# Kernel tuning notes

Hardware: AMD Instinct MI355X
Metric: run time of the kernel (lower is better)

Reference implementation:

```python
import jax, jax.numpy as jnp
import numpy as np

B, S, D, H, MULT = 4, 2048, 768, 12, 4
HD = D // H
EPS = 1e-6


def _ln(x, g, b):
    mu = jnp.mean(x, axis=-1, keepdims=True)
    var = jnp.var(x, axis=-1, keepdims=True)
    return (x - mu) * jax.lax.rsqrt(var + EPS) * g + b


def setup_inputs() -> dict:
    key = jax.random.key(0)
    ks = jax.random.split(key, 12)
    sd = 0.02
    inp = {
        "x": jax.random.normal(ks[0], (B, S, D), dtype=jnp.float32),
        "mask": jnp.ones((B, 1, 1, S), dtype=jnp.int32),
        "Wq": jax.random.normal(ks[1], (D, D), dtype=jnp.float32) * sd,
        "bq": jnp.zeros((D,), dtype=jnp.float32),
        "Wk": jax.random.normal(ks[2], (D, D), dtype=jnp.float32) * sd,
        "bk": jnp.zeros((D,), dtype=jnp.float32),
        "Wv": jax.random.normal(ks[3], (D, D), dtype=jnp.float32) * sd,
        "bv": jnp.zeros((D,), dtype=jnp.float32),
        "Wo": jax.random.normal(ks[4], (D, D), dtype=jnp.float32) * sd,
        "bo": jnp.zeros((D,), dtype=jnp.float32),
        "W1": jax.random.normal(ks[5], (D, MULT * D), dtype=jnp.float32) * sd,
        "b1": jnp.zeros((MULT * D,), dtype=jnp.float32),
        "W2": jax.random.normal(ks[6], (MULT * D, D), dtype=jnp.float32) * sd,
        "b2": jnp.zeros((D,), dtype=jnp.float32),
        "g1": jnp.ones((D,), dtype=jnp.float32),
        "be1": jnp.zeros((D,), dtype=jnp.float32),
        "g2": jnp.ones((D,), dtype=jnp.float32),
        "be2": jnp.zeros((D,), dtype=jnp.float32),
    }
    return inp


def reference(x, mask, Wq, bq, Wk, bk, Wv, bv, Wo, bo, W1, b1, W2, b2, g1, be1, g2, be2):
    scale = HD ** -0.5
    # projections -> [B,H,S,HD]
    q = (x @ Wq + bq).reshape(B, S, H, HD).transpose(0, 2, 1, 3)
    k = (x @ Wk + bk).reshape(B, S, H, HD).transpose(0, 2, 1, 3)
    v = (x @ Wv + bv).reshape(B, S, H, HD).transpose(0, 2, 1, 3)
    scores = jnp.einsum("bhqd,bhkd->bhqk", q, k) * scale
    scores = jnp.where(mask == 0, -jnp.inf, scores)
    attn = jax.nn.softmax(scores, axis=-1)
    out = jnp.einsum("bhqk,bhkd->bhqd", attn, v)
    out = out.transpose(0, 2, 1, 3).reshape(B, S, D)
    mha = out @ Wo + bo
    # residual + LN
    h = _ln(mha + x, g1, be1)
    # FFN (dropout inactive in eval; GELU exact as torch nn.GELU default)
    ff = jax.nn.gelu(h @ W1 + b1, approximate=False) @ W2 + b2
    return _ln(ff + h, g2, be2)
```

## Files before the change

kernel.cpp:

```cpp
#include <hip/hip_runtime.h>
#include <hip/hip_bf16.h>
#include <math.h>

#define B_  4
#define S_  2048
#define D_  768
#define H_  12
#define HD_ 64
#define DF_ 3072
#define BS_ (B_*S_)

#define QSCALE 0.18033688011112042f

typedef __attribute__((ext_vector_type(8))) short short8;
typedef __attribute__((ext_vector_type(4))) float f32x4;
typedef __attribute__((ext_vector_type(4))) int  int4v;

__device__ __forceinline__ unsigned short f2b(float f){
    unsigned int x = __float_as_uint(f);
    return (unsigned short)((x + 0x7fffu + ((x >> 16) & 1u)) >> 16);
}

typedef __attribute__((address_space(1))) void gvoid_t;
typedef __attribute__((address_space(3))) void lvoid_t;
__device__ __forceinline__ void gload_lds16(const unsigned short* g, unsigned short* l){
    __builtin_amdgcn_global_load_lds((gvoid_t*)g, (lvoid_t*)l, 16, 0, 0);
}

__global__ __launch_bounds__(256) void prep_kernel(
    const float* __restrict__ x,
    const float* __restrict__ Wq, const float* __restrict__ Wk,
    const float* __restrict__ Wv, const float* __restrict__ Wo,
    const float* __restrict__ W1, const float* __restrict__ W2,
    const float* __restrict__ bq, const float* __restrict__ bk, const float* __restrict__ bv,
    unsigned short* __restrict__ xb, unsigned short* __restrict__ wqkvT,
    unsigned short* __restrict__ woT, unsigned short* __restrict__ w1T,
    unsigned short* __restrict__ w2T, float* __restrict__ bqkv)
{
    const int NCVT = (BS_*D_)/256;
    int bid = blockIdx.x;
    if (bid < NCVT){
        int i = bid*256 + threadIdx.x;
        xb[i] = f2b(x[i]);
        return;
    }
    bid -= NCVT;
    __shared__ float t[32][33];
    const float* src; unsigned short* dst; int K, N, bx, by;
    if (bid < 4*576){
        int wsel = bid / 576, tt = bid % 576;
        bx = tt % 24; by = tt / 24; K = D_; N = D_;
        src = (wsel==0)?Wq:(wsel==1)?Wk:(wsel==2)?Wv:Wo;
        dst = (wsel<3) ? (wqkvT + (size_t)wsel*D_*D_) : woT;
    } else if (bid < 4*576 + 2304){
        int tt = bid - 4*576; bx = tt % 96; by = tt / 96; K = D_; N = DF_; src = W1; dst = w1T;
    } else if (bid < 4*576 + 2*2304){
        int tt = bid - 4*576 - 2304; bx = tt % 24; by = tt / 24; K = DF_; N = D_; src = W2; dst = w2T;
    } else {
        int i = (bid - (4*576 + 2*2304))*256 + threadIdx.x;
        if (i < 3*D_) bqkv[i] = (i < D_) ? bq[i] : (i < 2*D_) ? bk[i-D_] : bv[i-2*D_];
        return;
    }
    int tx = threadIdx.x & 31, ty = threadIdx.x >> 5;
    #pragma unroll
    for (int i = 0; i < 4; ++i)
        t[ty + i*8][tx] = src[(size_t)(by*32 + ty + i*8) * N + bx*32 + tx];
    __syncthreads();
    #pragma unroll
    for (int i = 0; i < 4; ++i)
        dst[(size_t)(bx*32 + ty + i*8) * K + by*32 + tx] = f2b(t[tx][ty + i*8]);
}

__global__ __launch_bounds__(256, 3) void gemm_tn(
    const unsigned short* __restrict__ A,
    const unsigned short* __restrict__ Bt,
    const float* __restrict__ bias,
    float* __restrict__ Cf,
    unsigned short* __restrict__ Cb,
    unsigned short* __restrict__ vtg,
    int M, int N, int K, int klen, int act)
{
    __shared__ __align__(16) unsigned short As[128*32];
    __shared__ __align__(16) unsigned short Bs[128*32];

    const int tid  = threadIdx.x;
    const int bm   = blockIdx.y, bn = blockIdx.x, bz = blockIdx.z;
    const int w    = tid >> 6, lane = tid & 63;
    const int l16  = lane & 15, quad = lane >> 4;
    const int wm   = (w >> 1) * 64, wn = (w & 1) * 64;
    const int kbeg = bz * klen;

    const unsigned short* Abase = A  + (size_t)bm * 128 * K;
    const unsigned short* Bbase = Bt + (size_t)bn * 128 * K;

    f32x4 acc[4][4] = {};

    for (int kt = kbeg; kt < kbeg + klen; kt += 32){
        #pragma unroll
        for (int c0 = 0; c0 < 2; ++c0){
            int c = tid + c0 * 256;
            int row = c >> 2, q = c & 3;
            gload_lds16(Abase + (size_t)row * K + kt + q*8, As + c*8);
            gload_lds16(Bbase + (size_t)row * K + kt + q*8, Bs + c*8);
        }
        __syncthreads();

        short8 af[4], bf[4];
        #pragma unroll
        for (int mi = 0; mi < 4; ++mi) af[mi] = *(const short8*)&As[(wm + mi*16 + l16)*32 + quad*8];
        #pragma unroll
        for (int ni = 0; ni < 4; ++ni) bf[ni] = *(const short8*)&Bs[(wn + ni*16 + l16)*32 + quad*8];
        #pragma unroll
        for (int mi = 0; mi < 4; ++mi)
            #pragma unroll
            for (int ni = 0; ni < 4; ++ni)
                acc[mi][ni] = __builtin_amdgcn_mfma_f32_16x16x32_bf16(af[mi], bf[ni], acc[mi][ni], 0, 0, 0);
        __syncthreads();
    }

    if (act == 2 && bn >= 12){
        #pragma unroll
        for (int mi = 0; mi < 4; ++mi){
            int rowbase = bm*128 + wm + mi*16 + quad*4;
            int bidx = rowbase >> 11, s0 = rowbase & 2047;
            int sp = (s0 & ~31) | (((s0 >> 2) & 3) << 3) | (((s0 >> 4) & 1) << 2);
            #pragma unroll
            for (int ni = 0; ni < 4; ++ni){
                int col  = bn*128 + wn + ni*16 + l16;
                int hcol = col - 2*D_;
                int hh   = hcol >> 6, dd = hcol & 63;
                float bia = bias ? bias[col] : 0.f;
                unsigned long long pk = 0;
                #pragma unroll
                for (int r = 0; r < 4; ++r)
                    pk |= (unsigned long long)f2b(acc[mi][ni][r] + bia) << (16*r);
                *(unsigned long long*)(vtg + (((size_t)bidx*H_ + hh)*64 + dd)*2048 + sp) = pk;
            }
        }
        return;
    }

    float* Cfz = Cf ? (Cf + (size_t)bz * M * N) : nullptr;
    const bool addb = (bias != nullptr) && (bz == 0);
    #pragma unroll
    for (int mi = 0; mi < 4; ++mi){
        #pragma unroll
        for (int ni = 0; ni < 4; ++ni){
            int col = bn*128 + wn + ni*16 + l16;
            float bia = addb ? bias[col] : 0.f;
            #pragma unroll
            for (int r = 0; r < 4; ++r){
                int row = bm*128 + wm + mi*16 + quad*4 + r;
                float v = acc[mi][ni][r] + bia;
                if (act == 1){
                    float u = v * (0.7978845608028654f + 0.0356774081f * v * v);
                    float e = __builtin_amdgcn_exp2f(u * 2.885390081777927f);
                    v = 0.5f * v * (1.f + (1.f - 2.f / (e + 1.f)));
                } else if (act == 2 && col < D_) v *= QSCALE;
                size_t idx = (size_t)row * N + col;
                if (Cfz) Cfz[idx] = v;
                if (Cb) Cb[idx] = f2b(v);
            }
        }
    }
}

__global__ __launch_bounds__(256, 2) void attn_kernel(
    const unsigned short* __restrict__ qkv,
    const unsigned short* __restrict__ vtg,
    const int* __restrict__ mask,
    unsigned short* __restrict__ ctx)
{
    __shared__ __align__(16) unsigned short Kl[128*64];
    __shared__ __align__(16) unsigned short Vt[64*128];

    const int tid = threadIdx.x;
    const int bid = blockIdx.x;
    const int hid = bid % 48;
    const int qb  = bid / 48;
    const int h   = hid % H_;
    const int b   = hid / H_;
    const int w   = tid >> 6, lane = tid & 63;
    const int l16 = lane & 15, quad = lane >> 4;
    const int q0  = qb * 128 + w * 32;
    const size_t base = (size_t)b * S_;
    const int hoff = h * HD_;

    short8 qf[2][2];
    #pragma unroll
    for (int nq = 0; nq < 2; ++nq)
        #pragma unroll
        for (int kc = 0; kc < 2; ++kc)
            qf[nq][kc] = *(const short8*)(qkv + (base + q0 + nq*16 + l16)*2304 + hoff + kc*32 + quad*8);

    f32x4 o[2][4] = {};
    float l_s[2] = {0.f, 0.f};

    const unsigned short* vrow = vtg + ((size_t)(b*H_ + h) * 64) * 2048;

    for (int kt = 0; kt < S_/128; ++kt){
        __syncthreads();
        #pragma unroll
        for (int c0 = 0; c0 < 4; ++c0){
            int c = tid + c0*256;
            int rr = c >> 3, ch = c & 7;
            int sw = (ch ^ rr) & 7;
            gload_lds16(qkv + (base + kt*128 + rr)*2304 + D_ + hoff + sw*8, Kl + c*8);
            int d = c >> 4, pch = c & 15;
            int lch = (pch ^ d) & 15;
            gload_lds16(vrow + (size_t)d*2048 + kt*128 + lch*8, Vt + c*8);
        }
        __syncthreads();

        f32x4 sf[2][8] = {};
        #pragma unroll
        for (int kc = 0; kc < 2; ++kc){
            short8 kfr[8];
            #pragma unroll
            for (int mk = 0; mk < 8; ++mk)
                kfr[mk] = *(const short8*)&Kl[(mk*16 + l16)*64 + (((kc*4 + quad) ^ l16) & 7)*8];
            #pragma unroll
            for (int nq = 0; nq < 2; ++nq)
                #pragma unroll
                for (int mk = 0; mk < 8; ++mk)
                    sf[nq][mk] = __builtin_amdgcn_mfma_f32_16x16x32_bf16(kfr[mk], qf[nq][kc], sf[nq][mk], 0, 0, 0);
        }

        int mv0 = mask[b*S_ + kt*128 + lane];
        int mv1 = mask[b*S_ + kt*128 + 64 + lane];
        if (!__all((mv0 != 0) && (mv1 != 0))){
            #pragma unroll
            for (int mk = 0; mk < 8; ++mk)
                #pragma unroll
                for (int r = 0; r < 4; ++r)
                    if (mask[b*S_ + kt*128 + mk*16 + quad*4 + r] == 0){
                        sf[0][mk][r] = -1e30f; sf[1][mk][r] = -1e30f;
                    }
        }

        #pragma unroll
        for (int nq = 0; nq < 2; ++nq){
            float acc = 0.f;
            #pragma unroll
            for (int mk = 0; mk < 8; ++mk)
                #pragma unroll
                for (int r = 0; r < 4; ++r){
                    float p = __builtin_amdgcn_exp2f(sf[nq][mk][r]);
                    sf[nq][mk][r] = p; acc += p;
                }
            l_s[nq] += acc;
        }

        #pragma unroll
        for (int kc2 = 0; kc2 < 4; ++kc2){
            short8 pf[2];
            #pragma unroll
            for (int mi = 0; mi < 2; ++mi){
                union { unsigned int u[4]; short8 s; } pk;
                #pragma unroll
                for (int t = 0; t < 2; ++t){
                    int mk = kc2*2 + t;
                    pk.u[t*2+0] = __builtin_amdgcn_perm(__float_as_uint(sf[mi][mk][1]),
                                                        __float_as_uint(sf[mi][mk][0]), 0x07060302u);
                    pk.u[t*2+1] = __builtin_amdgcn_perm(__float_as_uint(sf[mi][mk][3]),
                                                        __float_as_uint(sf[mi][mk][2]), 0x07060302u);
                }
                pf[mi] = pk.s;
            }
            #pragma unroll
            for (int nt = 0; nt < 4; ++nt){
                int d = nt*16 + l16;
                short8 vf = *(const short8*)&Vt[d*128 + (((kc2*4 + quad) ^ l16) & 15)*8];
                #pragma unroll
                for (int mi = 0; mi < 2; ++mi)
                    o[mi][nt] = __builtin_amdgcn_mfma_f32_16x16x32_bf16(pf[mi], vf, o[mi][nt], 0, 0, 0);
            }
        }
    }

    #pragma unroll
    for (int nq = 0; nq < 2; ++nq){
        l_s[nq] += __shfl_xor(l_s[nq], 16);
        l_s[nq] += __shfl_xor(l_s[nq], 32);
    }
    #pragma unroll
    for (int mi = 0; mi < 2; ++mi){
        float linv[4];
        #pragma unroll
        for (int r = 0; r < 4; ++r)
            linv[r] = 1.f / __shfl(l_s[mi], quad*4 + r);
        #pragma unroll
        for (int nt = 0; nt < 4; ++nt)
            #pragma unroll
            for (int r = 0; r < 4; ++r){
                int qrow = q0 + mi*16 + quad*4 + r;
                ctx[(base + qrow)*D_ + hoff + nt*16 + l16] = f2b(o[mi][nt][r] * linv[r]);
            }
    }
}

__global__ __launch_bounds__(256) void ln_kernel(
    const float* __restrict__ inp, const float* __restrict__ inp2,
    const float* __restrict__ res,
    const float* __restrict__ g, const float* __restrict__ be,
    float* __restrict__ outf, unsigned short* __restrict__ outb)
{
    const int row = blockIdx.x;
    const int tid = threadIdx.x;
    const float* ip = inp + (size_t)row * D_;
    const float* rp = res + (size_t)row * D_;
    const float* ip2 = inp2 ? inp2 + (size_t)row * D_ : nullptr;

    float v[3], s = 0.f, ss = 0.f;
    #pragma unroll
    for (int i = 0; i < 3; ++i){
        int c = tid + i*256;
        float x = ip[c] + rp[c];
        if (ip2) x += ip2[c];
        v[i] = x; s += x; ss += x * x;
    }
    #pragma unroll
    for (int d = 1; d < 64; d <<= 1){ s += __shfl_xor(s, d); ss += __shfl_xor(ss, d); }
    __shared__ float rs[4], rss[4];
    int w = tid >> 6;
    if ((tid & 63) == 0){ rs[w] = s; rss[w] = ss; }
    __syncthreads();
    s  = rs[0] + rs[1] + rs[2] + rs[3];
    ss = rss[0] + rss[1] + rss[2] + rss[3];
    float mu   = s * (1.f / 768.f);
    float var  = ss * (1.f / 768.f) - mu * mu;
    float rstd = rsqrtf(var + 1e-6f);
    #pragma unroll
    for (int i = 0; i < 3; ++i){
        int c = tid + i*256;
        float y = (v[i] - mu) * rstd * g[c] + be[c];
        if (outf) outf[(size_t)row * D_ + c] = y;
        if (outb) outb[(size_t)row * D_ + c] = f2b(y);
    }
}

extern "C" void kernel_launch(void* const* d_in, const int* in_sizes, int n_in,
                              void* d_out, int out_size, void* d_ws, size_t ws_size,
                              hipStream_t stream)
{
    const float* x    = (const float*)d_in[0];
    const int*   mask = (const int*)  d_in[1];
    const float* Wq   = (const float*)d_in[2];
    const float* bq   = (const float*)d_in[3];
    const float* Wk   = (const float*)d_in[4];
    const float* bk   = (const float*)d_in[5];
    const float* Wv   = (const float*)d_in[6];
    const float* bv   = (const float*)d_in[7];
    const float* Wo   = (const float*)d_in[8];
    const float* bo   = (const float*)d_in[9];
    const float* W1   = (const float*)d_in[10];
    const float* b1   = (const float*)d_in[11];
    const float* W2   = (const float*)d_in[12];
    const float* b2   = (const float*)d_in[13];
    const float* g1   = (const float*)d_in[14];
    const float* be1  = (const float*)d_in[15];
    const float* g2   = (const float*)d_in[16];
    const float* be2  = (const float*)d_in[17];
    float* out = (float*)d_out;
    (void)in_sizes; (void)n_in; (void)out_size; (void)ws_size;

    char* ws = (char*)d_ws;
    const size_t n_x = (size_t)BS_ * D_;

    size_t off = 0;
    auto take = [&](size_t bytes){ size_t o = off; off += (bytes + 255) & ~(size_t)255; return o; };
    unsigned short* xb    = (unsigned short*)(ws + take(n_x * 2));
    unsigned short* hb    = xb;
    unsigned short* wqkvT = (unsigned short*)(ws + take((size_t)3*D_*D_ * 2));
    unsigned short* woT   = (unsigned short*)(ws + take((size_t)D_*D_ * 2));
    unsigned short* w1T   = (unsigned short*)(ws + take((size_t)D_*DF_ * 2));
    unsigned short* w2T   = (unsigned short*)(ws + take((size_t)D_*DF_ * 2));
    float*          bqkv  = (float*)(ws + take((size_t)3*D_ * 4));
    size_t big = take((size_t)BS_ * 2304 * 2 + n_x * 2);
    unsigned short* qkvb = (unsigned short*)(ws + big);
    unsigned short* ctxb = qkvb + (size_t)BS_ * 2304;
    unsigned short* ff1b = qkvb;
    float* pf32 = (float*)(ws + take(2 * n_x * 4));
    float* mhaf = pf32;
    float* ff2f = pf32;
    size_t hfo = take(n_x * 4);
    float* hf = (float*)(ws + hfo);
    unsigned short* vtg = (unsigned short*)(ws + hfo);

    prep_kernel<<<24576 + 3*2304 + 9, 256, 0, stream>>>(
        x, Wq, Wk, Wv, Wo, W1, W2, bq, bk, bv,
        xb, wqkvT, woT, w1T, w2T, bqkv);

    dim3 blk(256);
    gemm_tn<<<dim3(18, 64, 1), blk, 0, stream>>>(xb, wqkvT, bqkv, nullptr, qkvb, vtg, BS_, 3*D_, D_, D_, 2);
    attn_kernel<<<B_ * H_ * (S_/128), blk, 0, stream>>>(qkvb, vtg, mask, ctxb);
    gemm_tn<<<dim3(6, 64, 2), blk, 0, stream>>>(ctxb, woT, bo, mhaf, nullptr, nullptr, BS_, D_, D_, D_/2, 0);
    ln_kernel<<<BS_, blk, 0, stream>>>(mhaf, mhaf + n_x, x, g1, be1, hf, hb);
    gemm_tn<<<dim3(24, 64, 1), blk, 0, stream>>>(hb, w1T, b1, nullptr, ff1b, nullptr, BS_, DF_, D_, D_, 1);
    gemm_tn<<<dim3(6, 64, 2), blk, 0, stream>>>(ff1b, w2T, b2, ff2f, nullptr, nullptr, BS_, D_, DF_, DF_/2, 0);
    ln_kernel<<<BS_, blk, 0, stream>>>(ff2f, ff2f + n_x, hf, g2, be2, out, nullptr);
}
```

Before: 453.3 us.

## Deepen GEMM K-tile with swizzle, restructure attention to 512 threads, drop fp32 LN residual

The GEMM now stages a 64-wide K tile with an XOR-swizzled LDS layout, halving the barrier count per K step and avoiding bank conflicts. The attention kernel uses 8 waves of 16 queries each and interleaves score, exp and PV per 32-key chunk, which lowers register pressure so more waves can be resident. The second LayerNorm reads its residual from the bf16 copy of h instead of a separate fp32 buffer, which removes one fp32 write and read but makes the residual slightly less precise.

```diff
diff --git a/kernel.cpp b/kernel.cpp
--- a/kernel.cpp
+++ b/kernel.cpp
@@ -19,6 +19,9 @@
 __device__ __forceinline__ unsigned short f2b(float f){
     unsigned int x = __float_as_uint(f);
     return (unsigned short)((x + 0x7fffu + ((x >> 16) & 1u)) >> 16);
+}
+__device__ __forceinline__ float b2f(unsigned short u){
+    return __uint_as_float(((unsigned int)u) << 16);
 }
 
 typedef __attribute__((address_space(1))) void gvoid_t;
@@ -80,8 +83,8 @@
     unsigned short* __restrict__ vtg,
     int M, int N, int K, int klen, int act)
 {
-    __shared__ __align__(16) unsigned short As[128*32];
-    __shared__ __align__(16) unsigned short Bs[128*32];
+    __shared__ __align__(16) unsigned short As[128*64];
+    __shared__ __align__(16) unsigned short Bs[128*64];
 
     const int tid  = threadIdx.x;
     const int bm   = blockIdx.y, bn = blockIdx.x, bz = blockIdx.z;
@@ -95,26 +98,32 @@
 
     f32x4 acc[4][4] = {};
 
-    for (int kt = kbeg; kt < kbeg + klen; kt += 32){
-        #pragma unroll
-        for (int c0 = 0; c0 < 2; ++c0){
+    for (int kt = kbeg; kt < kbeg + klen; kt += 64){
+        #pragma unroll
+        for (int c0 = 0; c0 < 4; ++c0){
             int c = tid + c0 * 256;
-            int row = c >> 2, q = c & 3;
-            gload_lds16(Abase + (size_t)row * K + kt + q*8, As + c*8);
-            gload_lds16(Bbase + (size_t)row * K + kt + q*8, Bs + c*8);
+            int row = c >> 3, q = c & 7;
+            int sw = (q ^ row) & 7;
+            gload_lds16(Abase + (size_t)row * K + kt + sw*8, As + c*8);
+            gload_lds16(Bbase + (size_t)row * K + kt + sw*8, Bs + c*8);
         }
         __syncthreads();
 
-        short8 af[4], bf[4];
-        #pragma unroll
-        for (int mi = 0; mi < 4; ++mi) af[mi] = *(const short8*)&As[(wm + mi*16 + l16)*32 + quad*8];
-        #pragma unroll
-        for (int ni = 0; ni < 4; ++ni) bf[ni] = *(const short8*)&Bs[(wn + ni*16 + l16)*32 + quad*8];
-        #pragma unroll
-        for (int mi = 0; mi < 4; ++mi)
+        #pragma unroll
+        for (int kc = 0; kc < 2; ++kc){
+            short8 af[4], bf[4];
+            #pragma unroll
+            for (int mi = 0; mi < 4; ++mi)
+                af[mi] = *(const short8*)&As[(wm + mi*16 + l16)*64 + (((kc*4 + quad) ^ l16) & 7)*8];
             #pragma unroll
             for (int ni = 0; ni < 4; ++ni)
-                acc[mi][ni] = __builtin_amdgcn_mfma_f32_16x16x32_bf16(af[mi], bf[ni], acc[mi][ni], 0, 0, 0);
+                bf[ni] = *(const short8*)&Bs[(wn + ni*16 + l16)*64 + (((kc*4 + quad) ^ l16) & 7)*8];
+            #pragma unroll
+            for (int mi = 0; mi < 4; ++mi)
+                #pragma unroll
+                for (int ni = 0; ni < 4; ++ni)
+                    acc[mi][ni] = __builtin_amdgcn_mfma_f32_16x16x32_bf16(af[mi], bf[ni], acc[mi][ni], 0, 0, 0);
+        }
         __syncthreads();
     }
 
@@ -165,7 +174,7 @@
     }
 }
 
-__global__ __launch_bounds__(256, 2) void attn_kernel(
+__global__ __launch_bounds__(512, 6) void attn_kernel(
     const unsigned short* __restrict__ qkv,
     const unsigned short* __restrict__ vtg,
     const int* __restrict__ mask,
@@ -182,27 +191,25 @@
     const int b   = hid / H_;
     const int w   = tid >> 6, lane = tid & 63;
     const int l16 = lane & 15, quad = lane >> 4;
-    const int q0  = qb * 128 + w * 32;
+    const int q0  = qb * 128 + w * 16;
     const size_t base = (size_t)b * S_;
     const int hoff = h * HD_;
 
-    short8 qf[2][2];
-    #pragma unroll
-    for (int nq = 0; nq < 2; ++nq)
-        #pragma unroll
-        for (int kc = 0; kc < 2; ++kc)
-            qf[nq][kc] = *(const short8*)(qkv + (base + q0 + nq*16 + l16)*2304 + hoff + kc*32 + quad*8);
-
-    f32x4 o[2][4] = {};
-    float l_s[2] = {0.f, 0.f};
+    short8 qf[2];
+    #pragma unroll
+    for (int kc = 0; kc < 2; ++kc)
+        qf[kc] = *(const short8*)(qkv + (base + q0 + l16)*2304 + hoff + kc*32 + quad*8);
+
+    f32x4 o[4] = {};
+    float l_s = 0.f;
 
     const unsigned short* vrow = vtg + ((size_t)(b*H_ + h) * 64) * 2048;
 
     for (int kt = 0; kt < S_/128; ++kt){
         __syncthreads();
         #pragma unroll
-        for (int c0 = 0; c0 < 4; ++c0){
-            int c = tid + c0*256;
+        for (int c0 = 0; c0 < 2; ++c0){
+            int c = tid + c0*512;
             int rr = c >> 3, ch = c & 7;
             int sw = (ch ^ rr) & 7;
             gload_lds16(qkv + (base + kt*128 + rr)*2304 + D_ + hoff + sw*8, Kl + c*8);
@@ -212,111 +219,83 @@
         }
         __syncthreads();
 
-        f32x4 sf[2][8] = {};
-        #pragma unroll
-        for (int kc = 0; kc < 2; ++kc){
-            short8 kfr[8];
-            #pragma unroll
-            for (int mk = 0; mk < 8; ++mk)
-                kfr[mk] = *(const short8*)&Kl[(mk*16 + l16)*64 + (((kc*4 + quad) ^ l16) & 7)*8];
-            #pragma unroll
-            for (int nq = 0; nq < 2; ++nq)
-                #pragma unroll
-                for (int mk = 0; mk < 8; ++mk)
-                    sf[nq][mk] = __builtin_amdgcn_mfma_f32_16x16x32_bf16(kfr[mk], qf[nq][kc], sf[nq][mk], 0, 0, 0);
-        }
-
         int mv0 = mask[b*S_ + kt*128 + lane];
         int mv1 = mask[b*S_ + kt*128 + 64 + lane];
-        if (!__all((mv0 != 0) && (mv1 != 0))){
-            #pragma unroll
-            for (int mk = 0; mk < 8; ++mk)
+        const bool allok = __all((mv0 != 0) && (mv1 != 0));
+
+        #pragma unroll
+        for (int t = 0; t < 4; ++t){
+            f32x4 sf2[2] = {};
+            #pragma unroll
+            for (int kc = 0; kc < 2; ++kc){
+                int co = (((kc*4 + quad) ^ l16) & 7)*8;
+                short8 k0 = *(const short8*)&Kl[((2*t  )*16 + l16)*64 + co];
+                short8 k1 = *(const short8*)&Kl[((2*t+1)*16 + l16)*64 + co];
+                sf2[0] = __builtin_amdgcn_mfma_f32_16x16x32_bf16(k0, qf[kc], sf2[0], 0, 0, 0);
+                sf2[1] = __builtin_amdgcn_mfma_f32_16x16x32_bf16(k1, qf[kc], sf2[1], 0, 0, 0);
+            }
+            if (!allok){
                 #pragma unroll
-                for (int r = 0; r < 4; ++r)
-                    if (mask[b*S_ + kt*128 + mk*16 + quad*4 + r] == 0){
-                        sf[0][mk][r] = -1e30f; sf[1][mk][r] = -1e30f;
-                    }
-        }
-
-        #pragma unroll
-        for (int nq = 0; nq < 2; ++nq){
-            float acc = 0.f;
-            #pragma unroll
-            for (int mk = 0; mk < 8; ++mk)
+                for (int j = 0; j < 2; ++j)
+                    #pragma unroll
+                    for (int r = 0; r < 4; ++r)
+                        if (mask[b*S_ + kt*128 + (2*t+j)*16 + quad*4 + r] == 0)
+                            sf2[j][r] = -1e30f;
+            }
+            #pragma unroll
+            for (int j = 0; j < 2; ++j)
                 #pragma unroll
                 for (int r = 0; r < 4; ++r){
-                    float p = __builtin_amdgcn_exp2f(sf[nq][mk][r]);
-                    sf[nq][mk][r] = p; acc += p;
+                    float p = __builtin_amdgcn_exp2f(sf2[j][r]);
+                    sf2[j][r] = p; l_s += p;
                 }
-            l_s[nq] += acc;
-        }
-
-        #pragma unroll
-        for (int kc2 = 0; kc2 < 4; ++kc2){
-            short8 pf[2];
-            #pragma unroll
-            for (int mi = 0; mi < 2; ++mi){
-                union { unsigned int u[4]; short8 s; } pk;
-                #pragma unroll
-                for (int t = 0; t < 2; ++t){
-                    int mk = kc2*2 + t;
-                    pk.u[t*2+0] = __builtin_amdgcn_perm(__float_as_uint(sf[mi][mk][1]),
-                                                        __float_as_uint(sf[mi][mk][0]), 0x07060302u);
-                    pk.u[t*2+1] = __builtin_amdgcn_perm(__float_as_uint(sf[mi][mk][3]),
-                                                        __float_as_uint(sf[mi][mk][2]), 0x07060302u);
-                }
-                pf[mi] = pk.s;
-            }
+            union { unsigned int u[4]; short8 s; } pk;
+            pk.u[0] = __builtin_amdgcn_perm(__float_as_uint(sf2[0][1]), __float_as_uint(sf2[0][0]), 0x07060302u);
+            pk.u[1] = __builtin_amdgcn_perm(__float_as_uint(sf2[0][3]), __float_as_uint(sf2[0][2]), 0x07060302u);
+            pk.u[2] = __builtin_amdgcn_perm(__float_as_uint(sf2[1][1]), __float_as_uint(sf2[1][0]), 0x07060302u);
+            pk.u[3] = __builtin_amdgcn_perm(__float_as_uint(sf2[1][3]), __float_as_uint(sf2[1][2]), 0x07060302u);
             #pragma unroll
             for (int nt = 0; nt < 4; ++nt){
                 int d = nt*16 + l16;
-                short8 vf = *(const short8*)&Vt[d*128 + (((kc2*4 + quad) ^ l16) & 15)*8];
-                #pragma unroll
-                for (int mi = 0; mi < 2; ++mi)
-                    o[mi][nt] = __builtin_amdgcn_mfma_f32_16x16x32_bf16(pf[mi], vf, o[mi][nt], 0, 0, 0);
-            }
-        }
-    }
-
-    #pragma unroll
-    for (int nq = 0; nq < 2; ++nq){
-        l_s[nq] += __shfl_xor(l_s[nq], 16);
-        l_s[nq] += __shfl_xor(l_s[nq], 32);
-    }
-    #pragma unroll
-    for (int mi = 0; mi < 2; ++mi){
-        float linv[4];
-        #pragma unroll
-        for (int r = 0; r < 4; ++r)
-            linv[r] = 1.f / __shfl(l_s[mi], quad*4 + r);
-        #pragma unroll
-        for (int nt = 0; nt < 4; ++nt)
-            #pragma unroll
-            for (int r = 0; r < 4; ++r){
-                int qrow = q0 + mi*16 + quad*4 + r;
-                ctx[(base + qrow)*D_ + hoff + nt*16 + l16] = f2b(o[mi][nt][r] * linv[r]);
-            }
-    }
+                short8 vf = *(const short8*)&Vt[d*128 + (((t*4 + quad) ^ l16) & 15)*8];
+                o[nt] = __builtin_amdgcn_mfma_f32_16x16x32_bf16(pk.s, vf, o[nt], 0, 0, 0);
+            }
+        }
+    }
+
+    l_s += __shfl_xor(l_s, 16);
+    l_s += __shfl_xor(l_s, 32);
+    float linv[4];
+    #pragma unroll
+    for (int r = 0; r < 4; ++r)
+        linv[r] = 1.f / __shfl(l_s, quad*4 + r);
+    #pragma unroll
+    for (int nt = 0; nt < 4; ++nt)
+        #pragma unroll
+        for (int r = 0; r < 4; ++r){
+            int qrow = q0 + quad*4 + r;
+            ctx[(base + qrow)*D_ + hoff + nt*16 + l16] = f2b(o[nt][r] * linv[r]);
+        }
 }
 
 __global__ __launch_bounds__(256) void ln_kernel(
     const float* __restrict__ inp, const float* __restrict__ inp2,
-    const float* __restrict__ res,
+    const float* __restrict__ resf, const unsigned short* __restrict__ resb,
     const float* __restrict__ g, const float* __restrict__ be,
     float* __restrict__ outf, unsigned short* __restrict__ outb)
 {
     const int row = blockIdx.x;
     const int tid = threadIdx.x;
     const float* ip = inp + (size_t)row * D_;
-    const float* rp = res + (size_t)row * D_;
     const float* ip2 = inp2 ? inp2 + (size_t)row * D_ : nullptr;
 
     float v[3], s = 0.f, ss = 0.f;
     #pragma unroll
     for (int i = 0; i < 3; ++i){
         int c = tid + i*256;
-        float x = ip[c] + rp[c];
+        float x = ip[c];
         if (ip2) x += ip2[c];
+        x += resf ? resf[(size_t)row * D_ + c] : b2f(resb[(size_t)row * D_ + c]);
         v[i] = x; s += x; ss += x * x;
     }
     #pragma unroll
@@ -383,9 +362,7 @@
     float* pf32 = (float*)(ws + take(2 * n_x * 4));
     float* mhaf = pf32;
     float* ff2f = pf32;
-    size_t hfo = take(n_x * 4);
-    float* hf = (float*)(ws + hfo);
-    unsigned short* vtg = (unsigned short*)(ws + hfo);
+    unsigned short* vtg = (unsigned short*)(ws + take(n_x * 2));
 
     prep_kernel<<<24576 + 3*2304 + 9, 256, 0, stream>>>(
         x, Wq, Wk, Wv, Wo, W1, W2, bq, bk, bv,
@@ -393,10 +370,10 @@
 
     dim3 blk(256);
     gemm_tn<<<dim3(18, 64, 1), blk, 0, stream>>>(xb, wqkvT, bqkv, nullptr, qkvb, vtg, BS_, 3*D_, D_, D_, 2);
-    attn_kernel<<<B_ * H_ * (S_/128), blk, 0, stream>>>(qkvb, vtg, mask, ctxb);
+    attn_kernel<<<B_ * H_ * (S_/128), 512, 0, stream>>>(qkvb, vtg, mask, ctxb);
     gemm_tn<<<dim3(6, 64, 2), blk, 0, stream>>>(ctxb, woT, bo, mhaf, nullptr, nullptr, BS_, D_, D_, D_/2, 0);
-    ln_kernel<<<BS_, blk, 0, stream>>>(mhaf, mhaf + n_x, x, g1, be1, hf, hb);
+    ln_kernel<<<BS_, blk, 0, stream>>>(mhaf, mhaf + n_x, x, nullptr, g1, be1, nullptr, hb);
     gemm_tn<<<dim3(24, 64, 1), blk, 0, stream>>>(hb, w1T, b1, nullptr, ff1b, nullptr, BS_, DF_, D_, D_, 1);
     gemm_tn<<<dim3(6, 64, 2), blk, 0, stream>>>(ff1b, w2T, b2, ff2f, nullptr, nullptr, BS_, D_, DF_, DF_/2, 0);
-    ln_kernel<<<BS_, blk, 0, stream>>>(ff2f, ff2f + n_x, hf, g2, be2, out, nullptr);
-}
+    ln_kernel<<<BS_, blk, 0, stream>>>(ff2f, ff2f + n_x, nullptr, hb, g2, be2, out, nullptr);
+}
```

Result: faster. 414.4 us (-8.6%).
